# Optimization experiments

Measured on AMD Instinct MI355X. Metric: run time of the kernel, lower is better.

## Reference

```python
import jax, jax.numpy as jnp
import numpy as np

N = 20000      # nodes
E = 320000     # edges (before self loops)
IN = 128       # in_channels
HID = 256      # hidden_channels
HEADS = 8
C = HID // HEADS  # 32 per-head dim
L = 4          # num_gat_layers
BN_EPS = 1e-5
LN_EPS = 1e-5


def setup_inputs() -> dict:
    key = jax.random.key(0)
    ks = iter(jax.random.split(key, 64))
    def rn(shape, s=0.05):
        return jax.random.normal(next(ks), shape, jnp.float32) * s
    inp = {
        'x': jax.random.normal(next(ks), (N, IN), jnp.float32),
        'edge_index': jax.random.randint(next(ks), (2, E), 0, N),
        # FeatureMLP
        'mlp_w1': rn((IN, HID)), 'mlp_b1': jnp.zeros((HID,), jnp.float32),
        'bn1_g': jnp.ones((HID,), jnp.float32), 'bn1_b': jnp.zeros((HID,), jnp.float32),
        'mlp_w2': rn((HID, HID)), 'mlp_b2': jnp.zeros((HID,), jnp.float32),
        'bn2_g': jnp.ones((HID,), jnp.float32), 'bn2_b': jnp.zeros((HID,), jnp.float32),
        'mlp_w3': rn((HID, HID)), 'mlp_b3': jnp.zeros((HID,), jnp.float32),
        # stacked GATv2 layer params [L, ...]
        'gat_wl': rn((L, HID, HID)), 'gat_bl': jnp.zeros((L, HID), jnp.float32),
        'gat_wr': rn((L, HID, HID)), 'gat_br': jnp.zeros((L, HID), jnp.float32),
        'gat_att': rn((L, HEADS, C)), 'gat_bias': jnp.zeros((L, HID), jnp.float32),
        'ln_g': jnp.ones((L, HID), jnp.float32), 'ln_b': jnp.zeros((L, HID), jnp.float32),
        'head_w1': rn((2 * HID, HID)), 'head_b1': jnp.zeros((HID,), jnp.float32),
        'hbn1_g': jnp.ones((HID,), jnp.float32), 'hbn1_b': jnp.zeros((HID,), jnp.float32),
        'head_w2': rn((HID, HID // 2)), 'head_b2': jnp.zeros((HID // 2,), jnp.float32),
        'hbn2_g': jnp.ones((HID // 2,), jnp.float32), 'hbn2_b': jnp.zeros((HID // 2,), jnp.float32),
        'head_w3': rn((HID // 2, HID // 4)), 'head_b3': jnp.zeros((HID // 4,), jnp.float32),
        'head_w4': rn((HID // 4, 1)), 'head_b4': jnp.zeros((1,), jnp.float32),
    }
    return inp


def _lrelu01(v):
    return jax.nn.leaky_relu(v, 0.1)


def _bn_eval(v, g, b):
    # eval-mode BatchNorm1d with running_mean=0, running_var=1
    return v * (g / jnp.sqrt(1.0 + BN_EPS)) + b


def _layernorm(v, g, b):
    mu = jnp.mean(v, axis=-1, keepdims=True)
    var = jnp.mean((v - mu) ** 2, axis=-1, keepdims=True)
    return (v - mu) / jnp.sqrt(var + LN_EPS) * g + b


def _gatv2(x, src, dst, Wl, bl, Wr, br, att, bias):
    n = x.shape[0]
    xl = (x @ Wl + bl).reshape(n, HEADS, C)   # source transform
    xr = (x @ Wr + br).reshape(n, HEADS, C)   # target transform
    # per-edge attention logits (GATv2): a . LeakyReLU(x_l[src] + x_r[dst])
    e = jax.nn.leaky_relu(xl[src] + xr[dst], 0.2)          # [E, H, C]
    logits = jnp.einsum('ehc,hc->eh', e, att)               # [E, H]
    # segment softmax over destination nodes
    m = jax.ops.segment_max(logits, dst, num_segments=n)    # [N, H]
    a = jnp.exp(logits - m[dst])
    s = jax.ops.segment_sum(a, dst, num_segments=n)
    alpha = a / (s[dst] + 1e-16)                            # [E, H]
    out = jax.ops.segment_sum(xl[src] * alpha[:, :, None], dst, num_segments=n)
    return out.reshape(n, HID) + bias


def _forward(x, mlp_w1, mlp_b1, bn1_g, bn1_b, mlp_w2, mlp_b2, bn2_g, bn2_b,
             mlp_w3, mlp_b3, gat_wl, gat_bl, gat_wr, gat_br, gat_att, gat_bias,
             ln_g, ln_b, head_w1, head_b1, hbn1_g, hbn1_b, head_w2, head_b2,
             hbn2_g, hbn2_b, head_w3, head_b3, head_w4, head_b4, edge_index):
    n = x.shape[0]
    # FeatureMLP (eval: dropout off)
    h = _lrelu01(_bn_eval(x @ mlp_w1 + mlp_b1, bn1_g, bn1_b))
    h = _lrelu01(_bn_eval(h @ mlp_w2 + mlp_b2, bn2_g, bn2_b))
    x_mlp = h @ mlp_w3 + mlp_b3
    # add self loops
    loop = jnp.arange(n)
    src = jnp.concatenate([edge_index[0], loop])
    dst = jnp.concatenate([edge_index[1], loop])
    g = x_mlp
    for i in range(L):
        res = g
        o = _gatv2(g, src, dst, gat_wl[i], gat_bl[i], gat_wr[i], gat_br[i],
                   gat_att[i], gat_bias[i])
        o = _lrelu01(_layernorm(o, ln_g[i], ln_b[i]))
        g = o + res
    xc = jnp.concatenate([x_mlp, g], axis=1)                # [N, 2*HID]
    h = _lrelu01(_bn_eval(xc @ head_w1 + head_b1, hbn1_g, hbn1_b))
    h = _lrelu01(_bn_eval(h @ head_w2 + head_b2, hbn2_g, hbn2_b))
    h = _lrelu01(h @ head_w3 + head_b3)
    return h @ head_w4 + head_b4                            # [N, 1]


def reference(x, edge_index, mlp_w1, mlp_b1, bn1_g, bn1_b, mlp_w2, mlp_b2,
              bn2_g, bn2_b, mlp_w3, mlp_b3, gat_wl, gat_bl, gat_wr, gat_br,
              gat_att, gat_bias, ln_g, ln_b, head_w1, head_b1, hbn1_g, hbn1_b,
              head_w2, head_b2, hbn2_g, hbn2_b, head_w3, head_b3, head_w4, head_b4):
    return _forward(x, mlp_w1, mlp_b1, bn1_g, bn1_b, mlp_w2, mlp_b2, bn2_g,
                    bn2_b, mlp_w3, mlp_b3, gat_wl, gat_bl, gat_wr, gat_br,
                    gat_att, gat_bias, ln_g, ln_b, head_w1, head_b1, hbn1_g,
                    hbn1_b, head_w2, head_b2, hbn2_g, hbn2_b, head_w3, head_b3,
                    head_w4, head_b4, edge_index)
```

## Files before the change

### kernel.cpp

```cpp
#include <hip/hip_runtime.h>
#include <hip/hip_bf16.h>

#define N_NODES 20000
#define E_EDGES 320000
#define E_TOT   (E_EDGES + N_NODES)
#define IN_CH   128
#define HID     256
#define HEADS   8
#define CPH     32

enum { EP_BIAS = 0, EP_BN_LRELU = 1, EP_LRELU = 2 };

typedef _Float16 f16;
typedef f16  f16x2 __attribute__((ext_vector_type(2)));
typedef f16  f16x4 __attribute__((ext_vector_type(4)));
typedef f16  f16x8 __attribute__((ext_vector_type(8)));
typedef float f32x2 __attribute__((ext_vector_type(2)));
typedef float f32x4 __attribute__((ext_vector_type(4)));

__device__ __forceinline__ f16x2 h2max(f16x2 a, f16x2 b) {
#if __has_builtin(__builtin_elementwise_max)
    return __builtin_elementwise_max(a, b);
#else
    f16x2 r; r[0] = a[0] > b[0] ? a[0] : b[0]; r[1] = a[1] > b[1] ? a[1] : b[1]; return r;
#endif
}
__device__ __forceinline__ float hdot2(f16x2 a, f16x2 b, float c) {
#if __has_builtin(__builtin_amdgcn_fdot2)
    return __builtin_amdgcn_fdot2(a, b, c, false);
#else
    return c + (float)a[0] * (float)b[0] + (float)a[1] * (float)b[1];
#endif
}
__device__ __forceinline__ float fexp2(float x) {
#if __has_builtin(__builtin_amdgcn_exp2f)
    return __builtin_amdgcn_exp2f(x);
#else
    return exp2f(x);
#endif
}

__device__ __forceinline__ size_t frag_idx(int row, int col, int KB) {
    int kb = col >> 6, ks = (col >> 5) & 1, q = (col >> 3) & 3, e = col & 7;
    return ((((size_t)(row >> 4) * KB + kb) * 2 + ks) << 9) + (((q << 4) | (row & 15)) << 3) + e;
}

struct WDesc { const float* src; f16* dst; int K; int Nc; int NTOT; int ct0; };
struct WDescs { WDesc d[14]; };

#define WPREP_BLKS (14 * 512)
#define CVT_BLKS   ((N_NODES * IN_CH) / 256)
#define DEG_BLKS   ((E_EDGES + 255) / 256)
#define ZERO_BLKS  ((N_NODES + 255) / 256)
#define PREP_BLKS  (WPREP_BLKS + CVT_BLKS + DEG_BLKS + ZERO_BLKS)

__global__ __launch_bounds__(256)
void prep_kernel(WDescs ds, const float* __restrict__ x, f16* __restrict__ x16,
                 const int* __restrict__ dstE, int* __restrict__ cnt, int* __restrict__ cur)
{
    const int bx = blockIdx.x;
    const int tid = threadIdx.x;
    if (bx < WPREP_BLKS) {
        WDesc w = ds.d[bx >> 9];
        int i = ((bx & 511) << 8) + tid;
        if (i < w.K * w.Nc) {
            int NT_local = w.Nc >> 4;
            int e  = i & 7;
            int l  = (i >> 3) & 63;
            int r  = i >> 9;
            int ct = r % NT_local;
            int q  = r / NT_local;
            int ks = q & 1;
            int kb = q >> 1;
            int n  = ct * 16 + (l & 15);
            int k  = kb * 64 + ks * 32 + ((l >> 4) << 3) + e;
            size_t di = (((size_t)(kb * 2 + ks) * w.NTOT + w.ct0 + ct) << 9) + (l << 3) + e;
            w.dst[di] = (f16)w.src[(size_t)k * w.Nc + n];
        }
    } else if (bx < WPREP_BLKS + CVT_BLKS) {
        int i = (bx - WPREP_BLKS) * 256 + tid;
        if (i < N_NODES * IN_CH) {
            int row = i / IN_CH, col = i - row * IN_CH;
            x16[frag_idx(row, col, 2)] = (f16)x[i];
        }
    } else if (bx < WPREP_BLKS + CVT_BLKS + DEG_BLKS) {
        int e = (bx - WPREP_BLKS - CVT_BLKS) * 256 + tid;
        if (e < E_EDGES) atomicAdd(&cnt[dstE[e]], 1);
    } else {
        int i = (bx - WPREP_BLKS - CVT_BLKS - DEG_BLKS) * 256 + tid;
        if (i < N_NODES) cur[i] = 0;
    }
}

template<int NT, int NTOT, int WAVES, int RT, int DOT, int OUTF>
__global__ __launch_bounds__(WAVES * 64)
void gemm_kernel(const f16* __restrict__ A1, int KB1,
                 const f16* __restrict__ A2, int KB2,
                 const f16* __restrict__ Wf,
                 const float* __restrict__ biasA,
                 const float* __restrict__ biasB,
                 const float* __restrict__ bng,
                 const float* __restrict__ bnb,
                 f16* __restrict__ out16A,
                 f16* __restrict__ out16B,
                 f16* __restrict__ dup16,
                 float* __restrict__ out32,
                 const float* __restrict__ dotw,
                 const float* __restrict__ dotb,
                 float* __restrict__ outdot,
                 int NcA, int KBo, int mode)
{
    __shared__ float red[DOT ? 16 : 1][DOT ? 65 : 1];
    const int tid  = threadIdx.x;
    const int wave = tid >> 6;
    const int lane = tid & 63;
    const int quad = lane >> 4;
    const int rb0 = blockIdx.x * RT;
    const int KBt = KB1 + KB2;

    f32x4 acc[RT][NT];
#pragma unroll
    for (int t = 0; t < RT; ++t)
#pragma unroll
        for (int j = 0; j < NT; ++j) acc[t][j] = (f32x4){0.f, 0.f, 0.f, 0.f};

#pragma unroll 2
    for (int kb = 0; kb < KBt; ++kb) {
#pragma unroll
        for (int ks = 0; ks < 2; ++ks) {
            f16x8 a[RT];
#pragma unroll
            for (int t = 0; t < RT; ++t) {
                const f16* ap = (kb < KB1)
                    ? A1 + (((((size_t)(rb0 + t)) * KB1 + kb) * 2 + ks) << 9) + (lane << 3)
                    : A2 + (((((size_t)(rb0 + t)) * KB2 + (kb - KB1)) * 2 + ks) << 9) + (lane << 3);
                a[t] = *(const f16x8*)ap;
            }
            const f16* bp = Wf + (((size_t)(kb * 2 + ks) * NTOT + wave * NT) << 9) + (lane << 3);
#pragma unroll
            for (int ct = 0; ct < NT; ++ct) {
                f16x8 b = *(const f16x8*)(bp + ((size_t)ct << 9));
#pragma unroll
                for (int t = 0; t < RT; ++t)
                    acc[t][ct] = __builtin_amdgcn_mfma_f32_16x16x32_f16(a[t], b, acc[t][ct], 0, 0, 0);
            }
        }
    }

    const int c0 = lane & 15;
    const int NcB = NTOT * 16 - NcA;
#pragma unroll
    for (int t = 0; t < RT; ++t) {
        const int r0 = (rb0 + t) * 16 + (quad << 2);
#pragma unroll
        for (int ct = 0; ct < NT; ++ct) {
            int col = (wave * NT + ct) * 16 + c0;
            bool isB = col >= NcA;
            int colL = isB ? col - NcA : col;
            float bv = isB ? biasB[colL] : biasA[colL];
            float sc = 1.f, sh = 0.f;
            if (mode == EP_BN_LRELU) {
                sc = bng[col] * rsqrtf(1.f + 1e-5f);
                sh = bnb[col];
            }
#pragma unroll
            for (int reg = 0; reg < 4; ++reg) {
                int row = r0 + reg;
                float v = acc[t][ct][reg] + bv;
                if (mode == EP_BN_LRELU) { v = v * sc + sh; v = v > 0.f ? v : 0.1f * v; }
                else if (mode == EP_LRELU) { v = v > 0.f ? v : 0.1f * v; }
                if (DOT) {
                    red[(quad << 2) + reg][col] = v * dotw[col];
                } else {
                    if (OUTF) {
                        size_t idx = frag_idx(row, col, KBo);
                        out16A[idx] = (f16)v;
                        if (dup16) dup16[idx] = (f16)v;
                        if (out32) out32[(size_t)row * NcA + col] = v;
                    } else {
                        f16* Cout = isB ? out16B : out16A;
                        int stride = isB ? NcB : NcA;
                        Cout[(size_t)row * stride + colL] = (f16)v;
                    }
                }
            }
        }
    }

    if (DOT) {
        __syncthreads();
        if (wave == 0) {
            int r = lane & 15, q = lane >> 4;
            float psum = 0.f;
#pragma unroll
            for (int j = 0; j < 16; ++j) psum += red[r][q * 16 + j];
            psum += __shfl_xor(psum, 16, 64);
            psum += __shfl_xor(psum, 32, 64);
            if (lane < 16) outdot[rb0 * 16 + r] = psum + dotb[0];
        }
    }
}

__global__ __launch_bounds__(1024)
void scan_kernel(const int* __restrict__ cnt, int* __restrict__ off) {
    __shared__ int wsum[16];
    const int tid = threadIdx.x, wv = tid >> 6, ln = tid & 63;
    const int base = tid * 20;
    int pre[20];
    int loc = 0;
#pragma unroll
    for (int j = 0; j < 20; ++j) {
        int i = base + j;
        int c = (i < N_NODES) ? cnt[i] + 1 : 0;
        pre[j] = loc;
        loc += c;
    }
    int s = loc;
#pragma unroll
    for (int d = 1; d < 64; d <<= 1) { int t = __shfl_up(s, d, 64); if (ln >= d) s += t; }
    if (ln == 63) wsum[wv] = s;
    __syncthreads();
    int woff = 0;
#pragma unroll
    for (int j = 0; j < 16; ++j) if (j < wv) woff += wsum[j];
    int excl = woff + s - loc;
#pragma unroll
    for (int j = 0; j < 20; ++j) {
        int i = base + j;
        if (i < N_NODES) off[i] = excl + pre[j];
    }
    if (tid == 1023) off[N_NODES] = woff + s;
}

__global__ void fill_kernel(const int* __restrict__ src, const int* __restrict__ dst,
                            const int* __restrict__ off, int* __restrict__ cur, int* __restrict__ csr) {
    int i = blockIdx.x * 256 + threadIdx.x;
    if (i < E_EDGES) {
        int d = dst[i];
        int pos = atomicAdd(&cur[d], 1);
        csr[off[d] + pos] = src[i];
    } else {
        int j = i - E_EDGES;
        if (j < N_NODES) csr[off[j + 1] - 1] = j;
    }
}

__global__ __launch_bounds__(256)
void gat_agg_kernel(const f16* __restrict__ xl, const f16* __restrict__ xr,
                    float* __restrict__ g, f16* __restrict__ g16,
                    const int* __restrict__ off, const int* __restrict__ csr,
                    const float* __restrict__ att,
                    const float* __restrict__ bias,
                    const float* __restrict__ lng,
                    const float* __restrict__ lnb)
{
    const int wv   = threadIdx.x >> 6;
    const int ln   = threadIdx.x & 63;
    const int half = ln >> 5;
    const int lp   = ln & 31;
    const int n    = blockIdx.x * 4 + wv;
    if (n >= N_NODES) return;

    const f16x8* xl8 = (const f16x8*)xl;
    f16x8 xrv = ((const f16x8*)xr)[n * 32 + lp];
    f16x2 xr0; xr0[0] = xrv[0]; xr0[1] = xrv[1];
    f16x2 xr1; xr1[0] = xrv[2]; xr1[1] = xrv[3];
    f16x2 xr2; xr2[0] = xrv[4]; xr2[1] = xrv[5];
    f16x2 xr3; xr3[0] = xrv[6]; xr3[1] = xrv[7];
    float4 af0 = ((const float4*)att)[lp * 2];
    float4 af1 = ((const float4*)att)[lp * 2 + 1];
    const float L2E = 1.44269504f;
    f16x2 av0; av0[0] = (f16)(af0.x * L2E); av0[1] = (f16)(af0.y * L2E);
    f16x2 av1; av1[0] = (f16)(af0.z * L2E); av1[1] = (f16)(af0.w * L2E);
    f16x2 av2; av2[0] = (f16)(af1.x * L2E); av2[1] = (f16)(af1.y * L2E);
    f16x2 av3; av3[0] = (f16)(af1.z * L2E); av3[1] = (f16)(af1.w * L2E);
    const f16x2 k02 = { (f16)0.2f, (f16)0.2f };

    float s = 0.f;
    float o0 = 0.f, o1 = 0.f, o2 = 0.f, o3 = 0.f, o4 = 0.f, o5 = 0.f, o6 = 0.f, o7 = 0.f;

    int p = off[n], end = off[n + 1];

    auto procv = [&](f16x8 xv, bool valid) {
        f16x2 x0; x0[0] = xv[0]; x0[1] = xv[1];
        f16x2 x1; x1[0] = xv[2]; x1[1] = xv[3];
        f16x2 x2; x2[0] = xv[4]; x2[1] = xv[5];
        f16x2 x3; x3[0] = xv[6]; x3[1] = xv[7];
        f16x2 v0 = x0 + xr0, v1 = x1 + xr1, v2 = x2 + xr2, v3 = x3 + xr3;
        v0 = h2max(v0, v0 * k02); v1 = h2max(v1, v1 * k02);
        v2 = h2max(v2, v2 * k02); v3 = h2max(v3, v3 * k02);
        float pr = hdot2(v0, av0, hdot2(v1, av1, hdot2(v2, av2, hdot2(v3, av3, 0.f))));
        pr += __shfl_xor(pr, 1, 64);
        pr += __shfl_xor(pr, 2, 64);
        float e = valid ? fexp2(pr) : 0.f;
        s += e;
        o0 = fmaf((float)xv[0], e, o0); o1 = fmaf((float)xv[1], e, o1);
        o2 = fmaf((float)xv[2], e, o2); o3 = fmaf((float)xv[3], e, o3);
        o4 = fmaf((float)xv[4], e, o4); o5 = fmaf((float)xv[5], e, o5);
        o6 = fmaf((float)xv[6], e, o6); o7 = fmaf((float)xv[7], e, o7);
    };
    auto proc = [&](int ep) {
        bool valid = ep < end;
        int sidx = csr[valid ? ep : end - 1];
        procv(xl8[(size_t)sidx * 32 + lp], valid);
    };

    for (; p + 8 <= end; p += 8) {
        int sA = csr[p +     half];
        int sB = csr[p + 2 + half];
        int sC = csr[p + 4 + half];
        int sD = csr[p + 6 + half];
        f16x8 rA = xl8[(size_t)sA * 32 + lp];
        f16x8 rB = xl8[(size_t)sB * 32 + lp];
        f16x8 rC = xl8[(size_t)sC * 32 + lp];
        f16x8 rD = xl8[(size_t)sD * 32 + lp];
        procv(rA, true); procv(rB, true); procv(rC, true); procv(rD, true);
    }
    for (; p + 4 <= end; p += 4) {
        int sA = csr[p +     half];
        int sB = csr[p + 2 + half];
        f16x8 rA = xl8[(size_t)sA * 32 + lp];
        f16x8 rB = xl8[(size_t)sB * 32 + lp];
        procv(rA, true); procv(rB, true);
    }
    for (; p < end; p += 2) proc(p + half);

    s  += __shfl_xor(s, 32, 64);
    o0 += __shfl_xor(o0, 32, 64); o1 += __shfl_xor(o1, 32, 64);
    o2 += __shfl_xor(o2, 32, 64); o3 += __shfl_xor(o3, 32, 64);
    o4 += __shfl_xor(o4, 32, 64); o5 += __shfl_xor(o5, 32, 64);
    o6 += __shfl_xor(o6, 32, 64); o7 += __shfl_xor(o7, 32, 64);

    const int lidx = lp * 2 + half;
    float q0 = half ? o4 : o0;
    float q1 = half ? o5 : o1;
    float q2 = half ? o6 : o2;
    float q3 = half ? o7 : o3;

    float inv = 1.f / (s + 1e-16f);
    float4 bi = ((const float4*)bias)[lidx];
    float y0 = q0 * inv + bi.x;
    float y1 = q1 * inv + bi.y;
    float y2 = q2 * inv + bi.z;
    float y3 = q3 * inv + bi.w;

    float s1 = y0 + y1 + y2 + y3;
    float s2 = y0 * y0 + y1 * y1 + y2 * y2 + y3 * y3;
#pragma unroll
    for (int d = 32; d; d >>= 1) { s1 += __shfl_xor(s1, d, 64); s2 += __shfl_xor(s2, d, 64); }
    float mu  = s1 * (1.f / HID);
    float ex2 = s2 * (1.f / HID);
    float rstd = rsqrtf(ex2 - mu * mu + 1e-5f);
    float4 lg = ((const float4*)lng)[lidx];
    float4 lb = ((const float4*)lnb)[lidx];
    float nv0 = (y0 - mu) * rstd * lg.x + lb.x; nv0 = nv0 > 0.f ? nv0 : 0.1f * nv0;
    float nv1 = (y1 - mu) * rstd * lg.y + lb.y; nv1 = nv1 > 0.f ? nv1 : 0.1f * nv1;
    float nv2 = (y2 - mu) * rstd * lg.z + lb.z; nv2 = nv2 > 0.f ? nv2 : 0.1f * nv2;
    float nv3 = (y3 - mu) * rstd * lg.w + lb.w; nv3 = nv3 > 0.f ? nv3 : 0.1f * nv3;

    float4 gv = ((const float4*)g)[n * 64 + lidx];
    float g0 = nv0 + gv.x, g1 = nv1 + gv.y, g2 = nv2 + gv.z, g3 = nv3 + gv.w;
    ((float4*)g)[n * 64 + lidx] = make_float4(g0, g1, g2, g3);
    f16x4 gh; gh[0] = (f16)g0; gh[1] = (f16)g1; gh[2] = (f16)g2; gh[3] = (f16)g3;
    *(f16x4*)&g16[frag_idx(n, 4 * lidx, 4)] = gh;
}

static inline size_t align_up(size_t v, size_t a) { return (v + a - 1) & ~(a - 1); }

extern "C" void kernel_launch(void* const* d_in, const int* in_sizes, int n_in,
                              void* d_out, int out_size, void* d_ws, size_t ws_size,
                              hipStream_t stream)
{
    const float* x      = (const float*)d_in[0];
    const int*   ei     = (const int*)d_in[1];
    const float* mlp_w1 = (const float*)d_in[2];
    const float* mlp_b1 = (const float*)d_in[3];
    const float* bn1_g  = (const float*)d_in[4];
    const float* bn1_b  = (const float*)d_in[5];
    const float* mlp_w2 = (const float*)d_in[6];
    const float* mlp_b2 = (const float*)d_in[7];
    const float* bn2_g  = (const float*)d_in[8];
    const float* bn2_b  = (const float*)d_in[9];
    const float* mlp_w3 = (const float*)d_in[10];
    const float* mlp_b3 = (const float*)d_in[11];
    const float* gat_wl = (const float*)d_in[12];
    const float* gat_bl = (const float*)d_in[13];
    const float* gat_wr = (const float*)d_in[14];
    const float* gat_br = (const float*)d_in[15];
    const float* gat_att  = (const float*)d_in[16];
    const float* gat_bias = (const float*)d_in[17];
    const float* ln_g   = (const float*)d_in[18];
    const float* ln_b   = (const float*)d_in[19];
    const float* head_w1 = (const float*)d_in[20];
    const float* head_b1 = (const float*)d_in[21];
    const float* hbn1_g  = (const float*)d_in[22];
    const float* hbn1_b  = (const float*)d_in[23];
    const float* head_w2 = (const float*)d_in[24];
    const float* head_b2 = (const float*)d_in[25];
    const float* hbn2_g  = (const float*)d_in[26];
    const float* hbn2_b  = (const float*)d_in[27];
    const float* head_w3 = (const float*)d_in[28];
    const float* head_b3 = (const float*)d_in[29];
    const float* head_w4 = (const float*)d_in[30];
    const float* head_b4 = (const float*)d_in[31];
    float* out = (float*)d_out;

    char* w = (char*)d_ws;
    size_t p = 0;
    int* off  = (int*)(w + p); p = align_up(p + (N_NODES + 1) * sizeof(int), 64);
    int* fill = (int*)(w + p); p = align_up(p + N_NODES * sizeof(int), 64);
    int* cur  = (int*)(w + p); p = align_up(p + N_NODES * sizeof(int), 64);
    int* csr  = (int*)(w + p); p = align_up(p + E_TOT * sizeof(int), 64);
    float* g32 = (float*)(w + p); p = align_up(p + (size_t)N_NODES * HID * 4, 64);
    auto halloc = [&](size_t elems) {
        f16* q = (f16*)(w + p);
        p = align_up(p + elems * 2, 1024);
        return q;
    };
    f16* x16     = halloc((size_t)N_NODES * IN_CH);
    f16* h1      = halloc((size_t)N_NODES * HID);
    f16* h2      = halloc((size_t)N_NODES * HID);
    f16* x_mlp16 = halloc((size_t)N_NODES * HID);
    f16* g16     = halloc((size_t)N_NODES * HID);
    f16* xl16    = halloc((size_t)N_NODES * HID);
    f16* xr16    = halloc((size_t)N_NODES * HID);
    f16* wt_mlp1 = halloc((size_t)IN_CH * HID);
    f16* wt_mlp2 = halloc((size_t)HID * HID);
    f16* wt_mlp3 = halloc((size_t)HID * HID);
    f16* wt_g[4];
    for (int i = 0; i < 4; ++i) wt_g[i] = halloc((size_t)HID * 2 * HID);
    f16* wt_h1 = halloc((size_t)2 * HID * HID);
    f16* wt_h2 = halloc((size_t)HID * (HID / 2));
    f16* wt_h3 = halloc((size_t)(HID / 2) * (HID / 4));
    (void)ws_size; (void)in_sizes; (void)n_in; (void)out_size;

    const int* e_src = ei;
    const int* e_dst = ei + E_EDGES;

    dim3 blk(256);
    dim3 gM625((N_NODES + 31) / 32);
    dim3 gM1250((N_NODES + 15) / 16);

    WDescs ds;
    ds.d[0]  = { mlp_w1, wt_mlp1, IN_CH, HID, 16, 0 };
    ds.d[1]  = { mlp_w2, wt_mlp2, HID, HID, 16, 0 };
    ds.d[2]  = { mlp_w3, wt_mlp3, HID, HID, 16, 0 };
    for (int i = 0; i < 4; ++i) {
        ds.d[3 + 2 * i] = { gat_wl + (size_t)i * HID * HID, wt_g[i], HID, HID, 32, 0 };
        ds.d[4 + 2 * i] = { gat_wr + (size_t)i * HID * HID, wt_g[i], HID, HID, 32, 16 };
    }
    ds.d[11] = { head_w1, wt_h1, 2 * HID, HID, 16, 0 };
    ds.d[12] = { head_w2, wt_h2, HID, HID / 2, 8, 0 };
    ds.d[13] = { head_w3, wt_h3, HID / 2, HID / 4, 4, 0 };

    hipMemsetAsync(fill, 0, N_NODES * sizeof(int), stream);
    prep_kernel<<<dim3(PREP_BLKS), blk, 0, stream>>>(ds, x, x16, e_dst, fill, cur);
    scan_kernel<<<1, 1024, 0, stream>>>(fill, off);
    fill_kernel<<<(E_TOT + 255) / 256, blk, 0, stream>>>(e_src, e_dst, off, cur, csr);

    gemm_kernel<2, 16, 8, 2, 0, 1><<<gM625, 512, 0, stream>>>(x16, 2, nullptr, 0, wt_mlp1, mlp_b1, mlp_b1,
        bn1_g, bn1_b, h1, nullptr, nullptr, nullptr, nullptr, nullptr, nullptr, HID, 4, EP_BN_LRELU);
    gemm_kernel<2, 16, 8, 2, 0, 1><<<gM625, 512, 0, stream>>>(h1, 4, nullptr, 0, wt_mlp2, mlp_b2, mlp_b2,
        bn2_g, bn2_b, h2, nullptr, nullptr, nullptr, nullptr, nullptr, nullptr, HID, 4, EP_BN_LRELU);
    gemm_kernel<2, 16, 8, 2, 0, 1><<<gM625, 512, 0, stream>>>(h2, 4, nullptr, 0, wt_mlp3, mlp_b3, mlp_b3,
        nullptr, nullptr, x_mlp16, nullptr, g16, g32, nullptr, nullptr, nullptr, HID, 4, EP_BIAS);

    for (int i = 0; i < 4; ++i) {
        gemm_kernel<4, 32, 8, 2, 0, 0><<<gM625, 512, 0, stream>>>(g16, 4, nullptr, 0, wt_g[i],
            gat_bl + i * HID, gat_br + i * HID, nullptr, nullptr,
            xl16, xr16, nullptr, nullptr, nullptr, nullptr, nullptr, HID, 0, EP_BIAS);
        gat_agg_kernel<<<(N_NODES + 3) / 4, blk, 0, stream>>>(xl16, xr16, g32, g16, off, csr,
                                                              gat_att + i * HID, gat_bias + i * HID,
                                                              ln_g + i * HID, ln_b + i * HID);
    }

    gemm_kernel<2, 16, 8, 2, 0, 1><<<gM625, 512, 0, stream>>>(x_mlp16, 4, g16, 4, wt_h1, head_b1, head_b1,
        hbn1_g, hbn1_b, h1, nullptr, nullptr, nullptr, nullptr, nullptr, nullptr, HID, 4, EP_BN_LRELU);
    gemm_kernel<1, 8, 8, 2, 0, 1><<<gM625, 512, 0, stream>>>(h1, 4, nullptr, 0, wt_h2, head_b2, head_b2,
        hbn2_g, hbn2_b, h2, nullptr, nullptr, nullptr, nullptr, nullptr, nullptr, HID / 2, 2, EP_BN_LRELU);
    gemm_kernel<1, 4, 4, 1, 1, 0><<<gM1250, 256, 0, stream>>>(h2, 2, nullptr, 0, wt_h3, head_b3, head_b3,
        nullptr, nullptr, nullptr, nullptr, nullptr, nullptr, head_w4, head_b4, out, HID / 4, 0, EP_LRELU);
}
```

Measured before the change: 448.4 us.

## Fuse head layers 2-4 into one kernel and unroll GAT gather by 16

Result: no change. 445.6 us (-0.6%).

```diff
diff --git a/kernel.cpp b/kernel.cpp
--- a/kernel.cpp
+++ b/kernel.cpp
@@ -201,6 +201,93 @@
     }
 }
 
+__global__ __launch_bounds__(512)
+void head23_kernel(const f16* __restrict__ h1,
+                   const f16* __restrict__ w2f,
+                   const float* __restrict__ b2,
+                   const float* __restrict__ bn2g, const float* __restrict__ bn2b,
+                   const f16* __restrict__ w3f,
+                   const float* __restrict__ b3,
+                   const float* __restrict__ w4, const float* __restrict__ b4,
+                   float* __restrict__ out)
+{
+    __shared__ f16  hs[32 * 136];
+    __shared__ float red[32][65];
+    const int tid  = threadIdx.x;
+    const int wave = tid >> 6;
+    const int lane = tid & 63;
+    const int quad = lane >> 4;
+    const int c0   = lane & 15;
+    const int rb0  = blockIdx.x * 2;
+
+    {
+        f32x4 acc[2];
+        acc[0] = (f32x4){0.f, 0.f, 0.f, 0.f};
+        acc[1] = (f32x4){0.f, 0.f, 0.f, 0.f};
+#pragma unroll
+        for (int kb = 0; kb < 4; ++kb) {
+#pragma unroll
+            for (int ks = 0; ks < 2; ++ks) {
+                f16x8 a0 = *(const f16x8*)(h1 + (((((size_t)rb0)     * 4 + kb) * 2 + ks) << 9) + (lane << 3));
+                f16x8 a1 = *(const f16x8*)(h1 + (((((size_t)rb0 + 1) * 4 + kb) * 2 + ks) << 9) + (lane << 3));
+                f16x8 b  = *(const f16x8*)(w2f + (((size_t)(kb * 2 + ks) * 8 + wave) << 9) + (lane << 3));
+                acc[0] = __builtin_amdgcn_mfma_f32_16x16x32_f16(a0, b, acc[0], 0, 0, 0);
+                acc[1] = __builtin_amdgcn_mfma_f32_16x16x32_f16(a1, b, acc[1], 0, 0, 0);
+            }
+        }
+        const int col = wave * 16 + c0;
+        const float sc = bn2g[col] * rsqrtf(1.f + 1e-5f);
+        const float sh = bn2b[col];
+        const float bv = b2[col];
+#pragma unroll
+        for (int t = 0; t < 2; ++t) {
+            const int r0 = t * 16 + (quad << 2);
+#pragma unroll
+            for (int reg = 0; reg < 4; ++reg) {
+                float v = acc[t][reg] + bv;
+                v = v * sc + sh;
+                v = v > 0.f ? v : 0.1f * v;
+                hs[(r0 + reg) * 136 + col] = (f16)v;
+            }
+        }
+    }
+    __syncthreads();
+
+    {
+        const int rbL = wave >> 2;
+        const int ct3 = wave & 3;
+        f32x4 acc = (f32x4){0.f, 0.f, 0.f, 0.f};
+#pragma unroll
+        for (int ksl = 0; ksl < 4; ++ksl) {
+            const int arow = rbL * 16 + (lane & 15);
+            f16x8 a = *(const f16x8*)&hs[arow * 136 + ksl * 32 + ((lane >> 4) << 3)];
+            f16x8 b = *(const f16x8*)(w3f + (((size_t)(ksl * 4 + ct3)) << 9) + (lane << 3));
+            acc = __builtin_amdgcn_mfma_f32_16x16x32_f16(a, b, acc, 0, 0, 0);
+        }
+        const int col = ct3 * 16 + c0;
+        const float wv = w4[col];
+        const float bv = b3[col];
+        const int r0 = rbL * 16 + (quad << 2);
+#pragma unroll
+        for (int reg = 0; reg < 4; ++reg) {
+            float v = acc[reg] + bv;
+            v = v > 0.f ? v : 0.1f * v;
+            red[r0 + reg][col] = v * wv;
+        }
+    }
+    __syncthreads();
+
+    {
+        const int row = wave * 4 + (lane >> 4);
+        float pr = red[row][c0] + red[row][c0 + 16] + red[row][c0 + 32] + red[row][c0 + 48];
+        pr += __shfl_xor(pr, 1, 64);
+        pr += __shfl_xor(pr, 2, 64);
+        pr += __shfl_xor(pr, 4, 64);
+        pr += __shfl_xor(pr, 8, 64);
+        if (c0 == 0) out[blockIdx.x * 32 + row] = pr + b4[0];
+    }
+}
+
 __global__ __launch_bounds__(1024)
 void scan_kernel(const int* __restrict__ cnt, int* __restrict__ off) {
     __shared__ int wsum[16];
@@ -305,6 +392,26 @@
         procv(xl8[(size_t)sidx * 32 + lp], valid);
     };
 
+    for (; p + 16 <= end; p += 16) {
+        int sA = csr[p +      half];
+        int sB = csr[p + 2  + half];
+        int sC = csr[p + 4  + half];
+        int sD = csr[p + 6  + half];
+        int sE = csr[p + 8  + half];
+        int sF = csr[p + 10 + half];
+        int sG = csr[p + 12 + half];
+        int sH = csr[p + 14 + half];
+        f16x8 rA = xl8[(size_t)sA * 32 + lp];
+        f16x8 rB = xl8[(size_t)sB * 32 + lp];
+        f16x8 rC = xl8[(size_t)sC * 32 + lp];
+        f16x8 rD = xl8[(size_t)sD * 32 + lp];
+        f16x8 rE = xl8[(size_t)sE * 32 + lp];
+        f16x8 rF = xl8[(size_t)sF * 32 + lp];
+        f16x8 rG = xl8[(size_t)sG * 32 + lp];
+        f16x8 rH = xl8[(size_t)sH * 32 + lp];
+        procv(rA, true); procv(rB, true); procv(rC, true); procv(rD, true);
+        procv(rE, true); procv(rF, true); procv(rG, true); procv(rH, true);
+    }
     for (; p + 8 <= end; p += 8) {
         int sA = csr[p +     half];
         int sB = csr[p + 2 + half];
@@ -439,7 +546,6 @@
 
     dim3 blk(256);
     dim3 gM625((N_NODES + 31) / 32);
-    dim3 gM1250((N_NODES + 15) / 16);
 
     WDescs ds;
     ds.d[0]  = { mlp_w1, wt_mlp1, IN_CH, HID, 16, 0 };
@@ -476,8 +582,6 @@
 
     gemm_kernel<2, 16, 8, 2, 0, 1><<<gM625, 512, 0, stream>>>(x_mlp16, 4, g16, 4, wt_h1, head_b1, head_b1,
         hbn1_g, hbn1_b, h1, nullptr, nullptr, nullptr, nullptr, nullptr, nullptr, HID, 4, EP_BN_LRELU);
-    gemm_kernel<1, 8, 8, 2, 0, 1><<<gM625, 512, 0, stream>>>(h1, 4, nullptr, 0, wt_h2, head_b2, head_b2,
-        hbn2_g, hbn2_b, h2, nullptr, nullptr, nullptr, nullptr, nullptr, nullptr, HID / 2, 2, EP_BN_LRELU);
-    gemm_kernel<1, 4, 4, 1, 1, 0><<<gM1250, 256, 0, stream>>>(h2, 2, nullptr, 0, wt_h3, head_b3, head_b3,
-        nullptr, nullptr, nullptr, nullptr, nullptr, nullptr, head_w4, head_b4, out, HID / 4, 0, EP_LRELU);
-}
+    head23_kernel<<<gM625, 512, 0, stream>>>(h1, wt_h2, head_b2, hbn2_g, hbn2_b,
+                                             wt_h3, head_b3, head_w4, head_b4, out);
+}
```
